# Kernel tuning notes

Measured on AMD Instinct MI355X. Metric: run time of the kernel, lower is better.

Reference implementation:

```python
import jax, jax.numpy as jnp
import numpy as np

EMBED_DIM = 768
NUM_HEADS = 12
HEAD_DIM = EMBED_DIM // NUM_HEADS


def setup_inputs() -> dict:
    key = jax.random.key(0)
    ks = jax.random.split(key, 9)
    B, S, D = 2, 2048, EMBED_DIM
    scale = 1.0 / np.sqrt(D)
    x = jax.random.normal(ks[0], (B, S, D), dtype=jnp.float32)
    Wq = jax.random.normal(ks[1], (D, D), dtype=jnp.float32) * scale
    bq = jax.random.normal(ks[2], (D,), dtype=jnp.float32) * 0.01
    Wk = jax.random.normal(ks[3], (D, D), dtype=jnp.float32) * scale
    bk = jax.random.normal(ks[4], (D,), dtype=jnp.float32) * 0.01
    Wv = jax.random.normal(ks[5], (D, D), dtype=jnp.float32) * scale
    bv = jax.random.normal(ks[6], (D,), dtype=jnp.float32) * 0.01
    Wo = jax.random.normal(ks[7], (D, D), dtype=jnp.float32) * scale
    bo = jax.random.normal(ks[8], (D,), dtype=jnp.float32) * 0.01
    return {"x": x, "Wq": Wq, "bq": bq, "Wk": Wk, "bk": bk,
            "Wv": Wv, "bv": bv, "Wo": Wo, "bo": bo}


def reference(x, Wq, bq, Wk, bk, Wv, bv, Wo, bo):
    B, S, D = x.shape
    H, hd = NUM_HEADS, HEAD_DIM
    # projections (torch Linear: x @ W^T + b; here W stored as (D,D) used directly)
    q = (x @ Wq + bq).reshape(B, S, H, hd).transpose(0, 2, 1, 3)  # (B,H,S,hd)
    k = (x @ Wk + bk).reshape(B, S, H, hd).transpose(0, 2, 1, 3)
    v = (x @ Wv + bv).reshape(B, S, H, hd).transpose(0, 2, 1, 3)
    scores = jnp.einsum('bhqd,bhkd->bhqk', q, k) / jnp.sqrt(jnp.float32(hd))
    attn = jax.nn.softmax(scores, axis=-1)                        # (B,H,S,S)
    out = jnp.einsum('bhqk,bhkd->bhqd', attn, v)                  # (B,H,S,hd)
    out = out.transpose(0, 2, 1, 3).reshape(B, S, D)
    return out @ Wo + bo
```

## Files before the change

kernel.cpp:

```cpp
#include <hip/hip_runtime.h>
#include <hip/hip_bf16.h>

#define NHEADS 12
#define HDIM 64
#define BATCH 2
#define SEQ 2048
#define DMODEL 768
#define MROWS (BATCH * SEQ)

typedef __bf16  bf16x8 __attribute__((ext_vector_type(8)));
typedef float   f32x4  __attribute__((ext_vector_type(4)));

__device__ inline unsigned short to_bf16(float f) {
    union { float f; unsigned u; } x; x.f = f;
    const unsigned r = x.u + 0x7FFFu + ((x.u >> 16) & 1u);
    return (unsigned short)(r >> 16);
}
__device__ inline float bf_to_f(unsigned short u) {
    union { unsigned u; float f; } x; x.u = ((unsigned)u) << 16; return x.f;
}

#define GLDS16(gsrc, ldst)                                                    \
    __builtin_amdgcn_global_load_lds(                                         \
        (const __attribute__((address_space(1))) void*)(gsrc),                \
        (__attribute__((address_space(3))) void*)(ldst), 16, 0, 0)

__global__ __launch_bounds__(256) void cvt_x(const float* __restrict__ in,
                                             unsigned short* __restrict__ out,
                                             int n4) {
    const int i = blockIdx.x * 256 + threadIdx.x;
    if (i < n4) {
        const float4 v = reinterpret_cast<const float4*>(in)[i];
        ushort4 o;
        o.x = to_bf16(v.x); o.y = to_bf16(v.y);
        o.z = to_bf16(v.z); o.w = to_bf16(v.w);
        reinterpret_cast<ushort4*>(out)[i] = o;
    }
}

__global__ __launch_bounds__(256) void cvt_wT(const float* __restrict__ Wq,
                                              const float* __restrict__ Wk,
                                              const float* __restrict__ Wv,
                                              const float* __restrict__ Wo,
                                              unsigned short* __restrict__ wt_all,
                                              unsigned short* __restrict__ wot) {
    const int z = blockIdx.z;
    const float* W = (z == 0) ? Wq : (z == 1) ? Wk : (z == 2) ? Wv : Wo;
    unsigned short* out = (z < 3) ? (wt_all + (size_t)z * DMODEL * DMODEL) : wot;

    __shared__ float tile[32][33];
    const int tx = threadIdx.x & 31, ty = threadIdx.x >> 5;
    const int nbase = blockIdx.x * 32, kbase = blockIdx.y * 32;

    #pragma unroll
    for (int p = 0; p < 4; ++p) {
        const int r = ty + p * 8;
        tile[r][tx] = W[(size_t)(kbase + r) * DMODEL + nbase + tx];
    }
    __syncthreads();
    #pragma unroll
    for (int p = 0; p < 4; ++p) {
        const int r = ty + p * 8;
        out[(size_t)(nbase + r) * DMODEL + kbase + tx] = to_bf16(tile[tx][r]);
    }
}

template <int OUT_MODE>
__global__ __launch_bounds__(256) void gemm_mfma(const unsigned short* __restrict__ A,
                                                 const unsigned short* __restrict__ Bt,
                                                 const float* __restrict__ bias,
                                                 void* __restrict__ outv,
                                                 float scale) {
    constexpr int K = DMODEL;
    __shared__ unsigned short As[128 * 32];
    __shared__ unsigned short Bs[128 * 32];

    const int t = threadIdx.x;
    const int lane = t & 63;
    const int w = t >> 6, wr = w >> 1, wc = w & 1;
    const int m0 = blockIdx.y * 128, n0 = blockIdx.x * 128;
    const int lr = lane & 15;
    const int kg = lane >> 4;

    const int row0 = t >> 2,        cp0 = t & 3;
    const int row1 = (t + 256) >> 2, cp1 = t & 3;
    const int c0 = cp0 ^ ((row0 >> 1) & 3);
    const int c1 = cp1 ^ ((row1 >> 1) & 3);
    unsigned short* asd0 = &As[(w * 64) * 8];
    unsigned short* asd1 = &As[(256 + w * 64) * 8];
    unsigned short* bsd0 = &Bs[(w * 64) * 8];
    unsigned short* bsd1 = &Bs[(256 + w * 64) * 8];

    f32x4 acc[4][4] = {};

    for (int k0 = 0; k0 < K; k0 += 32) {
        GLDS16(A  + (size_t)(m0 + row0) * K + k0 + c0 * 8, asd0);
        GLDS16(A  + (size_t)(m0 + row1) * K + k0 + c1 * 8, asd1);
        GLDS16(Bt + (size_t)(n0 + row0) * K + k0 + c0 * 8, bsd0);
        GLDS16(Bt + (size_t)(n0 + row1) * K + k0 + c1 * 8, bsd1);
        __syncthreads();

        bf16x8 af[4], bfr[4];
        #pragma unroll
        for (int i = 0; i < 4; ++i) {
            const int ar = wr * 64 + i * 16 + lr;
            af[i] = *reinterpret_cast<const bf16x8*>(
                &As[ar * 32 + ((kg ^ ((ar >> 1) & 3)) * 8)]);
            const int br = wc * 64 + i * 16 + lr;
            bfr[i] = *reinterpret_cast<const bf16x8*>(
                &Bs[br * 32 + ((kg ^ ((br >> 1) & 3)) * 8)]);
        }
        #pragma unroll
        for (int i = 0; i < 4; ++i)
            #pragma unroll
            for (int j = 0; j < 4; ++j)
                acc[i][j] = __builtin_amdgcn_mfma_f32_16x16x32_bf16(
                    af[i], bfr[j], acc[i][j], 0, 0, 0);
        __syncthreads();
    }

    const int mb = m0 + wr * 64, nb = n0 + wc * 64;
    #pragma unroll
    for (int i = 0; i < 4; ++i) {
        #pragma unroll
        for (int j = 0; j < 4; ++j) {
            const int col = nb + j * 16 + lr;
            const float bv = bias[col];
            if (OUT_MODE == 2) {
                ushort4 pk;
                #pragma unroll
                for (int q = 0; q < 4; ++q)
                    ((unsigned short*)&pk)[q] =
                        to_bf16((acc[i][j][q] + bv) * scale);
                const int r0 = mb + i * 16 + kg * 4;
                const int b = r0 >> 11, s = r0 & (SEQ - 1);
                const int h = col >> 6, d = col & (HDIM - 1);
                *reinterpret_cast<ushort4*>(
                    &((unsigned short*)outv)[(((size_t)(b * NHEADS + h)) * HDIM + d) * SEQ + s]) = pk;
            } else {
                #pragma unroll
                for (int q = 0; q < 4; ++q) {
                    const int row = mb + i * 16 + kg * 4 + q;
                    const float val = (acc[i][j][q] + bv) * scale;
                    if (OUT_MODE == 0) {
                        const int b = row >> 11, s = row & (SEQ - 1);
                        const int h = col >> 6, d = col & (HDIM - 1);
                        ((unsigned short*)outv)[(((size_t)(b * NHEADS + h)) * SEQ + s) * HDIM + d]
                            = to_bf16(val);
                    } else {
                        ((float*)outv)[(size_t)row * DMODEL + col] = val;
                    }
                }
            }
        }
    }
}

__global__ __launch_bounds__(256, 3) void flash_mfma(
        const unsigned short* __restrict__ Qg,
        const unsigned short* __restrict__ Kgl,
        const unsigned short* __restrict__ Vtg,
        unsigned short* __restrict__ Cctx) {
    __shared__ __align__(16) unsigned short k_s[64 * 72];
    __shared__ __align__(16) unsigned short v_s[64 * 72];
    __shared__ __align__(16) unsigned short p_s[4 * 16 * 72];

    const int t = threadIdx.x;
    const int lane = t & 63, w = t >> 6;
    const int lr = lane & 15, kg = lane >> 4;
    const int qb = blockIdx.x, bh = blockIdx.y;
    const size_t sbase = (size_t)bh * SEQ * HDIM;
    const size_t vtb   = (size_t)bh * HDIM * SEQ;

    const int q0 = qb * 64 + w * 16;
    const bf16x8 qf0 = *reinterpret_cast<const bf16x8*>(
        &Qg[sbase + (size_t)(q0 + lr) * HDIM + kg * 8]);
    const bf16x8 qf1 = *reinterpret_cast<const bf16x8*>(
        &Qg[sbase + (size_t)(q0 + lr) * HDIM + 32 + kg * 8]);

    const int sr = t >> 2, cst = t & 3;

    uint4 kr0, kr1, vr0, vr1;
    {
        const size_t ka = sbase + (size_t)sr * HDIM;
        kr0 = *reinterpret_cast<const uint4*>(&Kgl[ka + cst * 8]);
        kr1 = *reinterpret_cast<const uint4*>(&Kgl[ka + (cst + 4) * 8]);
        const size_t va = vtb + (size_t)sr * SEQ;
        vr0 = *reinterpret_cast<const uint4*>(&Vtg[va + cst * 8]);
        vr1 = *reinterpret_cast<const uint4*>(&Vtg[va + (cst + 4) * 8]);
    }

    f32x4 oa[4] = {};
    float m_run[4] = {-1e30f, -1e30f, -1e30f, -1e30f};
    float l_run[4] = {};

    const int NT = SEQ / 64;
    for (int kt = 0; kt < NT; ++kt) {
        __syncthreads();
        *reinterpret_cast<uint4*>(&k_s[sr * 72 + cst * 8])       = kr0;
        *reinterpret_cast<uint4*>(&k_s[sr * 72 + (cst + 4) * 8]) = kr1;
        *reinterpret_cast<uint4*>(&v_s[sr * 72 + cst * 8])       = vr0;
        *reinterpret_cast<uint4*>(&v_s[sr * 72 + (cst + 4) * 8]) = vr1;
        __syncthreads();
        if (kt + 1 < NT) {
            const size_t ka = sbase + (size_t)((kt + 1) * 64 + sr) * HDIM;
            kr0 = *reinterpret_cast<const uint4*>(&Kgl[ka + cst * 8]);
            kr1 = *reinterpret_cast<const uint4*>(&Kgl[ka + (cst + 4) * 8]);
            const size_t va = vtb + (size_t)sr * SEQ + (kt + 1) * 64;
            vr0 = *reinterpret_cast<const uint4*>(&Vtg[va + cst * 8]);
            vr1 = *reinterpret_cast<const uint4*>(&Vtg[va + (cst + 4) * 8]);
        }

        f32x4 st[4] = {};
        #pragma unroll
        for (int jk = 0; jk < 4; ++jk) {
            const bf16x8 kf0 = *reinterpret_cast<const bf16x8*>(
                &k_s[(jk * 16 + lr) * 72 + kg * 8]);
            const bf16x8 kf1 = *reinterpret_cast<const bf16x8*>(
                &k_s[(jk * 16 + lr) * 72 + 32 + kg * 8]);
            st[jk] = __builtin_amdgcn_mfma_f32_16x16x32_bf16(qf0, kf0, st[jk], 0, 0, 0);
            st[jk] = __builtin_amdgcn_mfma_f32_16x16x32_bf16(qf1, kf1, st[jk], 0, 0, 0);
        }

        float mx[4];
        #pragma unroll
        for (int q = 0; q < 4; ++q)
            mx[q] = fmaxf(fmaxf(st[0][q], st[1][q]), fmaxf(st[2][q], st[3][q]));
        #pragma unroll
        for (int s = 1; s < 16; s <<= 1)
            #pragma unroll
            for (int q = 0; q < 4; ++q)
                mx[q] = fmaxf(mx[q], __shfl_xor(mx[q], s));

        float f[4], rs[4];
        #pragma unroll
        for (int q = 0; q < 4; ++q) {
            const float mn = fmaxf(m_run[q], mx[q]);
            f[q] = __expf(m_run[q] - mn);
            m_run[q] = mn;
            rs[q] = 0.0f;
        }
        unsigned short pb[16];
        #pragma unroll
        for (int jk = 0; jk < 4; ++jk)
            #pragma unroll
            for (int q = 0; q < 4; ++q) {
                const unsigned short pbv = to_bf16(__expf(st[jk][q] - m_run[q]));
                pb[jk * 4 + q] = pbv;
                rs[q] += bf_to_f(pbv);
            }
        #pragma unroll
        for (int s = 1; s < 16; s <<= 1)
            #pragma unroll
            for (int q = 0; q < 4; ++q)
                rs[q] += __shfl_xor(rs[q], s);
        #pragma unroll
        for (int q = 0; q < 4; ++q)
            l_run[q] = l_run[q] * f[q] + rs[q];
        #pragma unroll
        for (int jd = 0; jd < 4; ++jd)
            #pragma unroll
            for (int q = 0; q < 4; ++q)
                oa[jd][q] *= f[q];

        const int pbase = w * (16 * 72);
        #pragma unroll
        for (int jk = 0; jk < 4; ++jk)
            #pragma unroll
            for (int q = 0; q < 4; ++q)
                p_s[pbase + (kg * 4 + q) * 72 + jk * 16 + lr] = pb[jk * 4 + q];
        const bf16x8 pf0 = *reinterpret_cast<const bf16x8*>(
            &p_s[pbase + lr * 72 + kg * 8]);
        const bf16x8 pf1 = *reinterpret_cast<const bf16x8*>(
            &p_s[pbase + lr * 72 + 32 + kg * 8]);

        #pragma unroll
        for (int jd = 0; jd < 4; ++jd) {
            const bf16x8 vf0 = *reinterpret_cast<const bf16x8*>(
                &v_s[(jd * 16 + lr) * 72 + kg * 8]);
            const bf16x8 vf1 = *reinterpret_cast<const bf16x8*>(
                &v_s[(jd * 16 + lr) * 72 + 32 + kg * 8]);
            oa[jd] = __builtin_amdgcn_mfma_f32_16x16x32_bf16(pf0, vf0, oa[jd], 0, 0, 0);
            oa[jd] = __builtin_amdgcn_mfma_f32_16x16x32_bf16(pf1, vf1, oa[jd], 0, 0, 0);
        }
    }

    const int b = bh / NHEADS, h = bh % NHEADS;
    #pragma unroll
    for (int q = 0; q < 4; ++q) {
        const float inv = 1.0f / l_run[q];
        const int s = q0 + kg * 4 + q;
        #pragma unroll
        for (int jd = 0; jd < 4; ++jd)
            Cctx[(size_t)(b * SEQ + s) * DMODEL + h * HDIM + jd * 16 + lr] =
                to_bf16(oa[jd][q] * inv);
    }
}

extern "C" void kernel_launch(void* const* d_in, const int* in_sizes, int n_in,
                              void* d_out, int out_size, void* d_ws, size_t ws_size,
                              hipStream_t stream) {
    const float* x  = (const float*)d_in[0];
    const float* Wq = (const float*)d_in[1];
    const float* bq = (const float*)d_in[2];
    const float* Wk = (const float*)d_in[3];
    const float* bk = (const float*)d_in[4];
    const float* Wv = (const float*)d_in[5];
    const float* bv = (const float*)d_in[6];
    const float* Wo = (const float*)d_in[7];
    const float* bo = (const float*)d_in[8];
    float* out = (float*)d_out;

    const size_t MD = (size_t)MROWS * DMODEL;
    const size_t W2 = (size_t)DMODEL * DMODEL;
    unsigned short* u = (unsigned short*)d_ws;
    unsigned short* x_bf   = u;
    unsigned short* q_bf   = u + MD;
    unsigned short* k_bf   = u + 2 * MD;
    unsigned short* vt_bf  = u + 3 * MD;
    unsigned short* c_bf   = u + 4 * MD;
    unsigned short* wt_all = u + 5 * MD;
    unsigned short* wot    = wt_all + 3 * W2;

    cvt_x<<<(int)(MD / 4 + 255) / 256, 256, 0, stream>>>(x, x_bf, (int)(MD / 4));
    cvt_wT<<<dim3(24, 24, 4), 256, 0, stream>>>(Wq, Wk, Wv, Wo, wt_all, wot);

    dim3 gg(DMODEL / 128, MROWS / 128);
    gemm_mfma<0><<<gg, 256, 0, stream>>>(x_bf, wt_all,          bq, q_bf, 0.125f);
    gemm_mfma<0><<<gg, 256, 0, stream>>>(x_bf, wt_all + W2,     bk, k_bf, 1.0f);
    gemm_mfma<2><<<gg, 256, 0, stream>>>(x_bf, wt_all + 2 * W2, bv, vt_bf, 1.0f);

    dim3 ga(SEQ / 64, BATCH * NHEADS);
    flash_mfma<<<ga, 256, 0, stream>>>(q_bf, k_bf, vt_bf, c_bf);

    gemm_mfma<1><<<gg, 256, 0, stream>>>(c_bf, wot, bo, out, 1.0f);
}
```

Baseline: 252.5 us.

## Fuse QKV GEMMs into one launch and move softmax row sums onto MFMA

Merges the three Q/K/V projection GEMMs into a single launch with a 3x wider grid, so x is shared across tiles and two launches go away. In the flash kernel, row sums are now computed by an MFMA against a ones vector instead of shuffle reductions, and P is packed with a paired bf16 conversion. It also adds s_setprio around the MFMA sections and raises the occupancy hint to 4 blocks per SM. The risks are register pressure from the tighter launch bound and a small precision change in the denominator accumulation.

```diff
diff --git a/kernel.cpp b/kernel.cpp
--- a/kernel.cpp
+++ b/kernel.cpp
@@ -16,8 +16,9 @@
     const unsigned r = x.u + 0x7FFFu + ((x.u >> 16) & 1u);
     return (unsigned short)(r >> 16);
 }
-__device__ inline float bf_to_f(unsigned short u) {
-    union { unsigned u; float f; } x; x.u = ((unsigned)u) << 16; return x.f;
+__device__ inline unsigned pack_bf16x2(float a, float b) {
+    const __hip_bfloat162 h = __float22bfloat162_rn(float2{a, b});
+    union { __hip_bfloat162 h; unsigned u; } c; c.h = h; return c.u;
 }
 
 #define GLDS16(gsrc, ldst)                                                    \
@@ -65,12 +66,14 @@
     }
 }
 
-template <int OUT_MODE>
-__global__ __launch_bounds__(256) void gemm_mfma(const unsigned short* __restrict__ A,
-                                                 const unsigned short* __restrict__ Bt,
-                                                 const float* __restrict__ bias,
-                                                 void* __restrict__ outv,
-                                                 float scale) {
+__global__ __launch_bounds__(256) void gemm_qkv(const unsigned short* __restrict__ A,
+                                                const unsigned short* __restrict__ Wt,
+                                                const float* __restrict__ bq,
+                                                const float* __restrict__ bk,
+                                                const float* __restrict__ bv,
+                                                unsigned short* __restrict__ q_bf,
+                                                unsigned short* __restrict__ k_bf,
+                                                unsigned short* __restrict__ vt_bf) {
     constexpr int K = DMODEL;
     __shared__ unsigned short As[128 * 32];
     __shared__ unsigned short Bs[128 * 32];
@@ -96,8 +99,8 @@
     for (int k0 = 0; k0 < K; k0 += 32) {
         GLDS16(A  + (size_t)(m0 + row0) * K + k0 + c0 * 8, asd0);
         GLDS16(A  + (size_t)(m0 + row1) * K + k0 + c1 * 8, asd1);
-        GLDS16(Bt + (size_t)(n0 + row0) * K + k0 + c0 * 8, bsd0);
-        GLDS16(Bt + (size_t)(n0 + row1) * K + k0 + c1 * 8, bsd1);
+        GLDS16(Wt + (size_t)(n0 + row0) * K + k0 + c0 * 8, bsd0);
+        GLDS16(Wt + (size_t)(n0 + row1) * K + k0 + c1 * 8, bsd1);
         __syncthreads();
 
         bf16x8 af[4], bfr[4];
@@ -119,6 +122,93 @@
         __syncthreads();
     }
 
+    const int seg = n0 / DMODEL;
+    const float scale = (seg == 0) ? 0.125f : 1.0f;
+    const float* bias = (seg == 0) ? bq : (seg == 1) ? bk : bv;
+    const int mb = m0 + wr * 64, nb = n0 - seg * DMODEL + wc * 64;
+
+    #pragma unroll
+    for (int i = 0; i < 4; ++i) {
+        #pragma unroll
+        for (int j = 0; j < 4; ++j) {
+            const int cl = nb + j * 16 + lr;
+            const float bv_ = bias[cl];
+            const int h = cl >> 6, d = cl & (HDIM - 1);
+            if (seg < 2) {
+                unsigned short* dst = (seg == 0) ? q_bf : k_bf;
+                #pragma unroll
+                for (int q = 0; q < 4; ++q) {
+                    const int row = mb + i * 16 + kg * 4 + q;
+                    const int b = row >> 11, s = row & (SEQ - 1);
+                    dst[(((size_t)(b * NHEADS + h)) * SEQ + s) * HDIM + d] =
+                        to_bf16((acc[i][j][q] + bv_) * scale);
+                }
+            } else {
+                ushort4 pk;
+                #pragma unroll
+                for (int q = 0; q < 4; ++q)
+                    ((unsigned short*)&pk)[q] = to_bf16(acc[i][j][q] + bv_);
+                const int r0 = mb + i * 16 + kg * 4;
+                const int b = r0 >> 11, s = r0 & (SEQ - 1);
+                *reinterpret_cast<ushort4*>(
+                    &vt_bf[(((size_t)(b * NHEADS + h)) * HDIM + d) * SEQ + s]) = pk;
+            }
+        }
+    }
+}
+
+__global__ __launch_bounds__(256) void gemm_out(const unsigned short* __restrict__ A,
+                                                const unsigned short* __restrict__ Bt,
+                                                const float* __restrict__ bias,
+                                                float* __restrict__ out) {
+    constexpr int K = DMODEL;
+    __shared__ unsigned short As[128 * 32];
+    __shared__ unsigned short Bs[128 * 32];
+
+    const int t = threadIdx.x;
+    const int lane = t & 63;
+    const int w = t >> 6, wr = w >> 1, wc = w & 1;
+    const int m0 = blockIdx.y * 128, n0 = blockIdx.x * 128;
+    const int lr = lane & 15;
+    const int kg = lane >> 4;
+
+    const int row0 = t >> 2,        cp0 = t & 3;
+    const int row1 = (t + 256) >> 2, cp1 = t & 3;
+    const int c0 = cp0 ^ ((row0 >> 1) & 3);
+    const int c1 = cp1 ^ ((row1 >> 1) & 3);
+    unsigned short* asd0 = &As[(w * 64) * 8];
+    unsigned short* asd1 = &As[(256 + w * 64) * 8];
+    unsigned short* bsd0 = &Bs[(w * 64) * 8];
+    unsigned short* bsd1 = &Bs[(256 + w * 64) * 8];
+
+    f32x4 acc[4][4] = {};
+
+    for (int k0 = 0; k0 < K; k0 += 32) {
+        GLDS16(A  + (size_t)(m0 + row0) * K + k0 + c0 * 8, asd0);
+        GLDS16(A  + (size_t)(m0 + row1) * K + k0 + c1 * 8, asd1);
+        GLDS16(Bt + (size_t)(n0 + row0) * K + k0 + c0 * 8, bsd0);
+        GLDS16(Bt + (size_t)(n0 + row1) * K + k0 + c1 * 8, bsd1);
+        __syncthreads();
+
+        bf16x8 af[4], bfr[4];
+        #pragma unroll
+        for (int i = 0; i < 4; ++i) {
+            const int ar = wr * 64 + i * 16 + lr;
+            af[i] = *reinterpret_cast<const bf16x8*>(
+                &As[ar * 32 + ((kg ^ ((ar >> 1) & 3)) * 8)]);
+            const int br = wc * 64 + i * 16 + lr;
+            bfr[i] = *reinterpret_cast<const bf16x8*>(
+                &Bs[br * 32 + ((kg ^ ((br >> 1) & 3)) * 8)]);
+        }
+        #pragma unroll
+        for (int i = 0; i < 4; ++i)
+            #pragma unroll
+            for (int j = 0; j < 4; ++j)
+                acc[i][j] = __builtin_amdgcn_mfma_f32_16x16x32_bf16(
+                    af[i], bfr[j], acc[i][j], 0, 0, 0);
+        __syncthreads();
+    }
+
     const int mb = m0 + wr * 64, nb = n0 + wc * 64;
     #pragma unroll
     for (int i = 0; i < 4; ++i) {
@@ -126,37 +216,16 @@
         for (int j = 0; j < 4; ++j) {
             const int col = nb + j * 16 + lr;
             const float bv = bias[col];
-            if (OUT_MODE == 2) {
-                ushort4 pk;
-                #pragma unroll
-                for (int q = 0; q < 4; ++q)
-                    ((unsigned short*)&pk)[q] =
-                        to_bf16((acc[i][j][q] + bv) * scale);
-                const int r0 = mb + i * 16 + kg * 4;
-                const int b = r0 >> 11, s = r0 & (SEQ - 1);
-                const int h = col >> 6, d = col & (HDIM - 1);
-                *reinterpret_cast<ushort4*>(
-                    &((unsigned short*)outv)[(((size_t)(b * NHEADS + h)) * HDIM + d) * SEQ + s]) = pk;
-            } else {
-                #pragma unroll
-                for (int q = 0; q < 4; ++q) {
-                    const int row = mb + i * 16 + kg * 4 + q;
-                    const float val = (acc[i][j][q] + bv) * scale;
-                    if (OUT_MODE == 0) {
-                        const int b = row >> 11, s = row & (SEQ - 1);
-                        const int h = col >> 6, d = col & (HDIM - 1);
-                        ((unsigned short*)outv)[(((size_t)(b * NHEADS + h)) * SEQ + s) * HDIM + d]
-                            = to_bf16(val);
-                    } else {
-                        ((float*)outv)[(size_t)row * DMODEL + col] = val;
-                    }
-                }
+            #pragma unroll
+            for (int q = 0; q < 4; ++q) {
+                const int row = mb + i * 16 + kg * 4 + q;
+                out[(size_t)row * DMODEL + col] = acc[i][j][q] + bv;
             }
         }
     }
 }
 
-__global__ __launch_bounds__(256, 3) void flash_mfma(
+__global__ __launch_bounds__(256, 4) void flash_mfma(
         const unsigned short* __restrict__ Qg,
         const unsigned short* __restrict__ Kgl,
         const unsigned short* __restrict__ Vtg,
@@ -177,6 +246,10 @@
         &Qg[sbase + (size_t)(q0 + lr) * HDIM + kg * 8]);
     const bf16x8 qf1 = *reinterpret_cast<const bf16x8*>(
         &Qg[sbase + (size_t)(q0 + lr) * HDIM + 32 + kg * 8]);
+
+    bf16x8 ones;
+    #pragma unroll
+    for (int i = 0; i < 8; ++i) ones[i] = (__bf16)1.0f;
 
     const int sr = t >> 2, cst = t & 3;
 
@@ -191,8 +264,8 @@
     }
 
     f32x4 oa[4] = {};
+    f32x4 l_acc = {};
     float m_run[4] = {-1e30f, -1e30f, -1e30f, -1e30f};
-    float l_run[4] = {};
 
     const int NT = SEQ / 64;
     for (int kt = 0; kt < NT; ++kt) {
@@ -212,6 +285,7 @@
         }
 
         f32x4 st[4] = {};
+        __builtin_amdgcn_s_setprio(1);
         #pragma unroll
         for (int jk = 0; jk < 4; ++jk) {
             const bf16x8 kf0 = *reinterpret_cast<const bf16x8*>(
@@ -221,6 +295,7 @@
             st[jk] = __builtin_amdgcn_mfma_f32_16x16x32_bf16(qf0, kf0, st[jk], 0, 0, 0);
             st[jk] = __builtin_amdgcn_mfma_f32_16x16x32_bf16(qf1, kf1, st[jk], 0, 0, 0);
         }
+        __builtin_amdgcn_s_setprio(0);
 
         float mx[4];
         #pragma unroll
@@ -232,31 +307,25 @@
             for (int q = 0; q < 4; ++q)
                 mx[q] = fmaxf(mx[q], __shfl_xor(mx[q], s));
 
-        float f[4], rs[4];
+        float f[4];
         #pragma unroll
         for (int q = 0; q < 4; ++q) {
             const float mn = fmaxf(m_run[q], mx[q]);
             f[q] = __expf(m_run[q] - mn);
             m_run[q] = mn;
-            rs[q] = 0.0f;
-        }
-        unsigned short pb[16];
-        #pragma unroll
-        for (int jk = 0; jk < 4; ++jk)
-            #pragma unroll
-            for (int q = 0; q < 4; ++q) {
-                const unsigned short pbv = to_bf16(__expf(st[jk][q] - m_run[q]));
-                pb[jk * 4 + q] = pbv;
-                rs[q] += bf_to_f(pbv);
-            }
-        #pragma unroll
-        for (int s = 1; s < 16; s <<= 1)
-            #pragma unroll
-            for (int q = 0; q < 4; ++q)
-                rs[q] += __shfl_xor(rs[q], s);
-        #pragma unroll
-        for (int q = 0; q < 4; ++q)
-            l_run[q] = l_run[q] * f[q] + rs[q];
+        }
+
+        unsigned pk01[4], pk23[4];
+        #pragma unroll
+        for (int jk = 0; jk < 4; ++jk) {
+            pk01[jk] = pack_bf16x2(__expf(st[jk][0] - m_run[0]),
+                                   __expf(st[jk][1] - m_run[1]));
+            pk23[jk] = pack_bf16x2(__expf(st[jk][2] - m_run[2]),
+                                   __expf(st[jk][3] - m_run[3]));
+        }
+
+        #pragma unroll
+        for (int q = 0; q < 4; ++q) l_acc[q] *= f[q];
         #pragma unroll
         for (int jd = 0; jd < 4; ++jd)
             #pragma unroll
@@ -265,15 +334,20 @@
 
         const int pbase = w * (16 * 72);
         #pragma unroll
-        for (int jk = 0; jk < 4; ++jk)
-            #pragma unroll
-            for (int q = 0; q < 4; ++q)
-                p_s[pbase + (kg * 4 + q) * 72 + jk * 16 + lr] = pb[jk * 4 + q];
+        for (int jk = 0; jk < 4; ++jk) {
+            p_s[pbase + (kg * 4 + 0) * 72 + jk * 16 + lr] = (unsigned short)(pk01[jk] & 0xFFFFu);
+            p_s[pbase + (kg * 4 + 1) * 72 + jk * 16 + lr] = (unsigned short)(pk01[jk] >> 16);
+            p_s[pbase + (kg * 4 + 2) * 72 + jk * 16 + lr] = (unsigned short)(pk23[jk] & 0xFFFFu);
+            p_s[pbase + (kg * 4 + 3) * 72 + jk * 16 + lr] = (unsigned short)(pk23[jk] >> 16);
+        }
         const bf16x8 pf0 = *reinterpret_cast<const bf16x8*>(
             &p_s[pbase + lr * 72 + kg * 8]);
         const bf16x8 pf1 = *reinterpret_cast<const bf16x8*>(
             &p_s[pbase + lr * 72 + 32 + kg * 8]);
 
+        __builtin_amdgcn_s_setprio(1);
+        l_acc = __builtin_amdgcn_mfma_f32_16x16x32_bf16(pf0, ones, l_acc, 0, 0, 0);
+        l_acc = __builtin_amdgcn_mfma_f32_16x16x32_bf16(pf1, ones, l_acc, 0, 0, 0);
         #pragma unroll
         for (int jd = 0; jd < 4; ++jd) {
             const bf16x8 vf0 = *reinterpret_cast<const bf16x8*>(
@@ -283,12 +357,13 @@
             oa[jd] = __builtin_amdgcn_mfma_f32_16x16x32_bf16(pf0, vf0, oa[jd], 0, 0, 0);
             oa[jd] = __builtin_amdgcn_mfma_f32_16x16x32_bf16(pf1, vf1, oa[jd], 0, 0, 0);
         }
+        __builtin_amdgcn_s_setprio(0);
     }
 
     const int b = bh / NHEADS, h = bh % NHEADS;
     #pragma unroll
     for (int q = 0; q < 4; ++q) {
-        const float inv = 1.0f / l_run[q];
+        const float inv = 1.0f / l_acc[q];
         const int s = q0 + kg * 4 + q;
         #pragma unroll
         for (int jd = 0; jd < 4; ++jd)
@@ -325,13 +400,12 @@
     cvt_x<<<(int)(MD / 4 + 255) / 256, 256, 0, stream>>>(x, x_bf, (int)(MD / 4));
     cvt_wT<<<dim3(24, 24, 4), 256, 0, stream>>>(Wq, Wk, Wv, Wo, wt_all, wot);
 
-    dim3 gg(DMODEL / 128, MROWS / 128);
-    gemm_mfma<0><<<gg, 256, 0, stream>>>(x_bf, wt_all,          bq, q_bf, 0.125f);
-    gemm_mfma<0><<<gg, 256, 0, stream>>>(x_bf, wt_all + W2,     bk, k_bf, 1.0f);
-    gemm_mfma<2><<<gg, 256, 0, stream>>>(x_bf, wt_all + 2 * W2, bv, vt_bf, 1.0f);
+    dim3 gq(3 * DMODEL / 128, MROWS / 128);
+    gemm_qkv<<<gq, 256, 0, stream>>>(x_bf, wt_all, bq, bk, bv, q_bf, k_bf, vt_bf);
 
     dim3 ga(SEQ / 64, BATCH * NHEADS);
     flash_mfma<<<ga, 256, 0, stream>>>(q_bf, k_bf, vt_bf, c_bf);
 
-    gemm_mfma<1><<<gg, 256, 0, stream>>>(c_bf, wot, bo, out, 1.0f);
-}
+    dim3 gg(DMODEL / 128, MROWS / 128);
+    gemm_out<<<gg, 256, 0, stream>>>(c_bf, wot, bo, out);
+}
```

Result: faster. 214.7 us (-15.0%).
